# Kernel optimization log

Measured on AMD Instinct MI355X. Metric: run time of the kernel, lower is better.

Reference implementation:

```python
import jax, jax.numpy as jnp
import numpy as np

N_NODES = 100000


def _sage_conv(x, src, dst, W_l, b, W_r):
    """PyG SAGEConv with mean aggregation: lin_l(mean_{j in N(i)} x_j) + lin_r(x_i).
    edge_index[0]=src (message source j), edge_index[1]=dst (target i)."""
    n = x.shape[0]
    # sum of neighbor features per target node, then divide by in-degree
    agg = jax.ops.segment_sum(x[src], dst, num_segments=n)  # [N, F]
    deg = jax.ops.segment_sum(jnp.ones_like(dst, dtype=x.dtype), dst, num_segments=n)
    agg = agg / jnp.maximum(deg, 1.0)[:, None]
    return agg @ W_l + b + x @ W_r


def setup_inputs() -> dict:
    key = jax.random.key(0)
    ks = jax.random.split(key, 8)
    in_c, hid, out = 128, 128, 2
    sc = lambda f: 1.0 / np.sqrt(f)
    x = jax.random.normal(ks[0], (N_NODES, in_c), dtype=jnp.float32)
    edge_index = jax.random.randint(ks[1], (2, 1600000), 0, N_NODES, dtype=jnp.int64)
    return {
        "x": x,
        "edge_index": edge_index,
        "W1_l": jax.random.normal(ks[2], (in_c, hid), dtype=jnp.float32) * sc(in_c),
        "b1": jnp.zeros((hid,), dtype=jnp.float32),
        "W1_r": jax.random.normal(ks[3], (in_c, hid), dtype=jnp.float32) * sc(in_c),
        "W2_l": jax.random.normal(ks[4], (hid, hid), dtype=jnp.float32) * sc(hid),
        "b2": jnp.zeros((hid,), dtype=jnp.float32),
        "W2_r": jax.random.normal(ks[5], (hid, hid), dtype=jnp.float32) * sc(hid),
        "W_fc": jax.random.normal(ks[6], (hid, out), dtype=jnp.float32) * sc(hid),
        "b_fc": jnp.zeros((out,), dtype=jnp.float32),
    }


def reference(x, edge_index, W1_l, b1, W1_r, W2_l, b2, W2_r, W_fc, b_fc):
    src, dst = edge_index[0], edge_index[1]
    # eval mode: dropout is identity
    h = jax.nn.relu(_sage_conv(x, src, dst, W1_l, b1, W1_r))
    h = jax.nn.relu(_sage_conv(h, src, dst, W2_l, b2, W2_r))
    return h @ W_fc + b_fc
```

## Files before the change

kernel.cpp:

```cpp
#include <hip/hip_runtime.h>

#define NF 128
#define SH 9
#define BNODES 512
#define MAXNB 256

typedef unsigned short u16;
typedef unsigned int u32;
using u16x4 = __attribute__((ext_vector_type(4))) u16;
using u16x8 = __attribute__((ext_vector_type(8))) u16;
using s16x8 = __attribute__((ext_vector_type(8))) short;
using f32x4 = __attribute__((ext_vector_type(4))) float;
using u32x4 = __attribute__((ext_vector_type(4))) u32;
using i32x4 = __attribute__((ext_vector_type(4))) int;

__device__ inline float b2f(u16 b) {
    union { u32 u; float f; } c; c.u = (u32)b << 16; return c.f;
}
__device__ inline u16 f2b(float f) {
    union { float f; u32 u; } c; c.f = f;
    u32 u = c.u;
    u += 0x7FFFu + ((u >> 16) & 1u);
    return (u16)(u >> 16);
}
__device__ inline u16x8 nt_load8(const u16* p) {
    u32x4 v = __builtin_nontemporal_load((const u32x4*)p);
    return *(u16x8*)&v;
}
__device__ inline void nt_store8(u16* p, u16x8 v) {
    __builtin_nontemporal_store(*(u32x4*)&v, (u32x4*)p);
}
__device__ inline int padded4(int d) { return (d + 3) & ~3; }

__global__ __launch_bounds__(256) void bhist_kernel(const int* __restrict__ dst,
                                                    int* __restrict__ bcnt, int E, int NB) {
    __shared__ int h[MAXNB];
    int t = threadIdx.x;
    h[t] = 0;
    __syncthreads();
    for (int e = blockIdx.x * 256 + t; e < E; e += gridDim.x * 256)
        atomicAdd(&h[__builtin_nontemporal_load(dst + e) >> SH], 1);
    __syncthreads();
    if (t < NB && h[t]) atomicAdd(&bcnt[t], h[t]);
}

__global__ __launch_bounds__(256) void bscan_kernel(const int* __restrict__ bcnt,
                                                    int* __restrict__ boff,
                                                    int* __restrict__ gcur, int NB, int E) {
    __shared__ int ss[256];
    int t = threadIdx.x;
    int v = (t < NB) ? bcnt[t] : 0;
    ss[t] = v; __syncthreads();
    for (int off = 1; off < 256; off <<= 1) {
        int u = (t >= off) ? ss[t - off] : 0;
        __syncthreads();
        ss[t] += u;
        __syncthreads();
    }
    int excl = ss[t] - v;
    if (t < NB) { boff[t] = excl; gcur[t] = excl; }
    if (t == 0) boff[NB] = E;
}

__global__ __launch_bounds__(256) void scatter_kernel(
    const int* __restrict__ src, const int* __restrict__ dst,
    int* __restrict__ gcur, u32* __restrict__ pairs, int E, int NB)
{
    __shared__ int hist[MAXNB];
    __shared__ int cstart[256];
    __shared__ int gbase[MAXNB];
    __shared__ u32 stage[4096];
    __shared__ u16 bmap[4096];
    int t = threadIdx.x;
    int base = blockIdx.x * 4096;

    hist[t] = 0;
    __syncthreads();

    u32 packed[16]; int bb[16]; int loff[16];
    #pragma unroll
    for (int j = 0; j < 16; j++) {
        int e = base + j * 256 + t;
        bb[j] = -1;
        if (e < E) {
            int d = __builtin_nontemporal_load(dst + e);
            int s = __builtin_nontemporal_load(src + e);
            int b = d >> SH;
            bb[j] = b;
            packed[j] = ((u32)(d & (BNODES - 1)) << 17) | (u32)s;
            loff[j] = atomicAdd(&hist[b], 1);
        }
    }
    __syncthreads();

    int hv = hist[t];
    cstart[t] = hv; __syncthreads();
    for (int off = 1; off < 256; off <<= 1) {
        int u = (t >= off) ? cstart[t - off] : 0;
        __syncthreads();
        cstart[t] += u;
        __syncthreads();
    }
    int excl = cstart[t] - hv;
    if (t < NB && hv > 0) gbase[t] = atomicAdd(&gcur[t], hv);
    __syncthreads();
    cstart[t] = excl;
    __syncthreads();

    #pragma unroll
    for (int j = 0; j < 16; j++) if (bb[j] >= 0) {
        int pos = cstart[bb[j]] + loff[j];
        stage[pos] = packed[j];
        bmap[pos] = (u16)bb[j];
    }
    __syncthreads();

    int total = min(4096, E - base);
    for (int k = t; k < total; k += 256) {
        u32 p = stage[k];
        int b = bmap[k];
        pairs[gbase[b] + (k - cstart[b])] = p;
    }
}

__global__ __launch_bounds__(256) void degb_kernel(const u32* __restrict__ pairs,
                                                   const int* __restrict__ boff,
                                                   int* __restrict__ deg, int n) {
    __shared__ int dl[BNODES];
    int b = blockIdx.x, t = threadIdx.x;
    for (int i = t; i < BNODES; i += 256) dl[i] = 0;
    __syncthreads();
    int s = boff[b], e = boff[b + 1];
    for (int k = s + t; k < e; k += 256)
        atomicAdd(&dl[__builtin_nontemporal_load(pairs + k) >> 17], 1);
    __syncthreads();
    int nb0 = b << SH;
    for (int i = t; i < BNODES; i += 256)
        if (nb0 + i < n) deg[nb0 + i] = dl[i];
}

__global__ __launch_bounds__(256) void scanA_kernel(const int* __restrict__ deg,
                                                    int* __restrict__ bsum, int n) {
    __shared__ int red[256];
    int t = threadIdx.x;
    int i0 = blockIdx.x * 1024 + t * 4;
    int s = 0;
    if (i0 + 3 < n) {
        int4 d = *(const int4*)(deg + i0);
        s = padded4(d.x) + padded4(d.y) + padded4(d.z) + padded4(d.w);
    } else {
        for (int j = 0; j < 4; j++) if (i0 + j < n) s += padded4(deg[i0 + j]);
    }
    red[t] = s; __syncthreads();
    for (int off = 128; off; off >>= 1) {
        if (t < off) red[t] += red[t + off];
        __syncthreads();
    }
    if (!t) bsum[blockIdx.x] = red[0];
}

__global__ __launch_bounds__(128) void scanB_kernel(int* __restrict__ bsum, int nb) {
    __shared__ int ss[128];
    int t = threadIdx.x;
    int v = (t < nb) ? bsum[t] : 0;
    ss[t] = v; __syncthreads();
    for (int off = 1; off < 128; off <<= 1) {
        int u = (t >= off) ? ss[t - off] : 0;
        __syncthreads();
        ss[t] += u;
        __syncthreads();
    }
    if (t < nb) bsum[t] = ss[t] - v;
}

__global__ __launch_bounds__(256) void scanC_kernel(const int* __restrict__ deg,
                                                    const int* __restrict__ bsum,
                                                    int* __restrict__ info,
                                                    int* __restrict__ adj, int n) {
    __shared__ int ss[256];
    int t = threadIdx.x;
    int i0 = blockIdx.x * 1024 + t * 4;
    int4 d = make_int4(0, 0, 0, 0);
    if (i0 + 3 < n) d = *(const int4*)(deg + i0);
    else {
        if (i0     < n) d.x = deg[i0];
        if (i0 + 1 < n) d.y = deg[i0 + 1];
        if (i0 + 2 < n) d.z = deg[i0 + 2];
        if (i0 + 3 < n) d.w = deg[i0 + 3];
    }
    int px = padded4(d.x), py = padded4(d.y), pz = padded4(d.z), pw = padded4(d.w);
    int s = px + py + pz + pw;
    ss[t] = s; __syncthreads();
    for (int off = 1; off < 256; off <<= 1) {
        int u = (t >= off) ? ss[t - off] : 0;
        __syncthreads();
        ss[t] += u;
        __syncthreads();
    }
    int b0 = bsum[blockIdx.x] + ss[t] - s;
    int b1 = b0 + px, b2 = b1 + py, b3 = b2 + pz;
    if (i0 + 3 < n) {
        i32x4 w0 = {b0, d.x, b1, d.y};
        i32x4 w1 = {b2, d.z, b3, d.w};
        ((i32x4*)info)[i0 / 2]     = w0;
        ((i32x4*)info)[i0 / 2 + 1] = w1;
    } else {
        if (i0     < n) { info[2 * i0]     = b0; info[2 * i0 + 1] = d.x; }
        if (i0 + 1 < n) { info[2 * i0 + 2] = b1; info[2 * i0 + 3] = d.y; }
        if (i0 + 2 < n) { info[2 * i0 + 4] = b2; info[2 * i0 + 5] = d.z; }
        if (i0 + 3 < n) { info[2 * i0 + 6] = b3; info[2 * i0 + 7] = d.w; }
    }
    if (i0     < n) for (int p = d.x; p < px; p++) adj[b0 + p] = n;
    if (i0 + 1 < n) for (int p = d.y; p < py; p++) adj[b1 + p] = n;
    if (i0 + 2 < n) for (int p = d.z; p < pz; p++) adj[b2 + p] = n;
    if (i0 + 3 < n) for (int p = d.w; p < pw; p++) adj[b3 + p] = n;
}

__global__ __launch_bounds__(256) void fill2_kernel(const u32* __restrict__ pairs,
                                                    const int* __restrict__ boff,
                                                    const int* __restrict__ info,
                                                    int* __restrict__ adj, int n) {
    __shared__ int begl[BNODES];
    __shared__ int curl[BNODES];
    int b = blockIdx.x, t = threadIdx.x;
    int nb0 = b << SH;
    for (int i = t; i < BNODES; i += 256) {
        int nd = nb0 + i;
        if (nd < n) begl[i] = info[2 * nd];
        curl[i] = 0;
    }
    __syncthreads();
    int s = boff[b], e = boff[b + 1];
    for (int k = s + t; k < e; k += 256) {
        u32 p = __builtin_nontemporal_load(pairs + k);
        int ld = p >> 17, sr = p & 0x1FFFF;
        int pos = atomicAdd(&curl[ld], 1);
        adj[begl[ld] + pos] = sr;
    }
}

__global__ __launch_bounds__(256) void cast_x_kernel(const float* __restrict__ x,
                                                     u16* __restrict__ xb, int n, int nr) {
    int i = blockIdx.x * 256 + threadIdx.x;
    if (i >= nr * (NF / 8)) return;
    int node = i >> 4, ch = i & 15;
    u16x8 o = (u16x8)0;
    if (node < n) {
        const float* p = x + (size_t)node * NF + ch * 8;
        f32x4 v0 = __builtin_nontemporal_load((const f32x4*)p);
        f32x4 v1 = __builtin_nontemporal_load((const f32x4*)(p + 4));
        o[0] = f2b(v0[0]); o[1] = f2b(v0[1]); o[2] = f2b(v0[2]); o[3] = f2b(v0[3]);
        o[4] = f2b(v1[0]); o[5] = f2b(v1[1]); o[6] = f2b(v1[2]); o[7] = f2b(v1[3]);
    }
    *(u16x8*)(xb + (size_t)node * NF + ch * 8) = o;
}

__global__ void cast_wt_kernel(const float* __restrict__ w0, const float* __restrict__ w1,
                               const float* __restrict__ w2, const float* __restrict__ w3,
                               u16* __restrict__ o0, u16* __restrict__ o1,
                               u16* __restrict__ o2, u16* __restrict__ o3) {
    int m = blockIdx.y;
    const float* w = (m == 0) ? w0 : (m == 1) ? w1 : (m == 2) ? w2 : w3;
    u16* o = (m == 0) ? o0 : (m == 1) ? o1 : (m == 2) ? o2 : o3;
    int i = blockIdx.x * 256 + threadIdx.x;
    int k = i >> 7, nc = i & 127;
    o[nc * NF + k] = f2b(w[k * NF + nc]);
}

__global__ __launch_bounds__(256) void gather_kernel(
    const u16* __restrict__ xb,
    const int* __restrict__ info,
    const int* __restrict__ adj,
    u16* __restrict__ agg,
    int n)
{
    int node = blockIdx.x * 16 + (threadIdx.x >> 4);
    if (node >= n) return;
    int lane = threadIdx.x & 15;
    const u16* xs = xb + lane * 8;

    int2 inf = *(const int2*)(info + 2 * node);
    int beg = inf.x, deg = inf.y;
    const i32x4* ap = (const i32x4*)(adj + beg);
    int ng = (deg + 3) >> 2;

    float a[8];
    #pragma unroll
    for (int j = 0; j < 8; j++) a[j] = 0.f;

#define ROW(nb) (*(const u16x8*)(xs + (size_t)(nb) * NF))

    i32x4 ia, ib;
    if (ng >= 2) {
        ia = __builtin_nontemporal_load(ap);
        ib = __builtin_nontemporal_load(ap + 1);
    }
    int g = 0;
    while (g + 2 <= ng) {
        i32x4 ca = ia, cb = ib;
        g += 2;
        if (g + 2 <= ng) {
            ia = __builtin_nontemporal_load(ap + g);
            ib = __builtin_nontemporal_load(ap + g + 1);
        }
        u16x8 v0 = ROW(ca[0]), v1 = ROW(ca[1]), v2 = ROW(ca[2]), v3 = ROW(ca[3]);
        u16x8 v4 = ROW(cb[0]), v5 = ROW(cb[1]), v6 = ROW(cb[2]), v7 = ROW(cb[3]);
        #pragma unroll
        for (int j = 0; j < 8; j++)
            a[j] += ((b2f(v0[j]) + b2f(v1[j])) + (b2f(v2[j]) + b2f(v3[j])))
                  + ((b2f(v4[j]) + b2f(v5[j])) + (b2f(v6[j]) + b2f(v7[j])));
    }
    if (g < ng) {
        i32x4 ca = __builtin_nontemporal_load(ap + g);
        u16x8 v0 = ROW(ca[0]), v1 = ROW(ca[1]), v2 = ROW(ca[2]), v3 = ROW(ca[3]);
        #pragma unroll
        for (int j = 0; j < 8; j++)
            a[j] += (b2f(v0[j]) + b2f(v1[j])) + (b2f(v2[j]) + b2f(v3[j]));
    }
#undef ROW

    float invd = 1.0f / fmaxf((float)deg, 1.0f);
    u16x8 o;
    #pragma unroll
    for (int j = 0; j < 8; j++) o[j] = f2b(a[j] * invd);
    *(u16x8*)(agg + (size_t)node * NF + lane * 8) = o;
}

template <bool FC>
__global__ __launch_bounds__(256) void sage_mfma_kernel(
    const u16* __restrict__ agg,
    const u16* __restrict__ selfb,
    const u16* __restrict__ Wtl,
    const u16* __restrict__ Wtr,
    const float* __restrict__ bias,
    const float* __restrict__ Wfc,
    const float* __restrict__ bfc,
    u16* __restrict__ hout,
    float* __restrict__ out,
    int n)
{
    constexpr int MT = 64;
    constexpr int LDK = 136;
    __shared__ u16 A_s[MT][LDK];
    __shared__ u16 W_s[NF][LDK];

    int t = threadIdx.x;
    int node0 = blockIdx.x * MT;

    #pragma unroll
    for (int i = 0; i < 8; i++) {
        int idx = t + i * 256;
        int row = idx >> 4, ch = idx & 15;
        *(u16x8*)&W_s[row][ch * 8] = ((const u16x8*)Wtl)[row * 16 + ch];
    }
    #pragma unroll
    for (int i = 0; i < 4; i++) {
        int idx = t + i * 256;
        int row = idx >> 4, ch = idx & 15;
        int node = node0 + row;
        u16x8 v = (u16x8)0;
        if (node < n) v = nt_load8(agg + (size_t)node * NF + ch * 8);
        *(u16x8*)&A_s[row][ch * 8] = v;
    }
    __syncthreads();

    int l = t & 63;
    int lr = l & 15;
    int lko = (l >> 4) * 8;
    int m0 = (t >> 6) * 16;

    f32x4 acc[8];
    #pragma unroll
    for (int f = 0; f < 8; f++) acc[f] = (f32x4)0.f;

    #pragma unroll
    for (int ks = 0; ks < NF; ks += 32) {
        s16x8 a = *(const s16x8*)&A_s[m0 + lr][ks + lko];
        #pragma unroll
        for (int f = 0; f < 8; f++) {
            s16x8 b = *(const s16x8*)&W_s[f * 16 + lr][ks + lko];
            acc[f] = __builtin_amdgcn_mfma_f32_16x16x32_bf16(a, b, acc[f], 0, 0, 0);
        }
    }
    __syncthreads();

    #pragma unroll
    for (int i = 0; i < 8; i++) {
        int idx = t + i * 256;
        int row = idx >> 4, ch = idx & 15;
        *(u16x8*)&W_s[row][ch * 8] = ((const u16x8*)Wtr)[row * 16 + ch];
    }
    #pragma unroll
    for (int i = 0; i < 4; i++) {
        int idx = t + i * 256;
        int row = idx >> 4, ch = idx & 15;
        int node = node0 + row;
        u16x8 v = (u16x8)0;
        if (node < n) v = nt_load8(selfb + (size_t)node * NF + ch * 8);
        *(u16x8*)&A_s[row][ch * 8] = v;
    }
    __syncthreads();

    #pragma unroll
    for (int ks = 0; ks < NF; ks += 32) {
        s16x8 a = *(const s16x8*)&A_s[m0 + lr][ks + lko];
        #pragma unroll
        for (int f = 0; f < 8; f++) {
            s16x8 b = *(const s16x8*)&W_s[f * 16 + lr][ks + lko];
            acc[f] = __builtin_amdgcn_mfma_f32_16x16x32_bf16(a, b, acc[f], 0, 0, 0);
        }
    }

    __syncthreads();
    int rowb = m0 + (l >> 4) * 4;
    #pragma unroll
    for (int f = 0; f < 8; f++) {
        float bc = bias[f * 16 + lr];
        #pragma unroll
        for (int r = 0; r < 4; r++) {
            float v = fmaxf(acc[f][r] + bc, 0.f);
            A_s[rowb + r][f * 16 + lr] = f2b(v);
        }
    }
    __syncthreads();

    if (!FC) {
        #pragma unroll
        for (int i = 0; i < 4; i++) {
            int idx = t + i * 256;
            int row = idx >> 4, ch = idx & 15;
            int node = node0 + row;
            if (node < n)
                nt_store8(hout + (size_t)node * NF + ch * 8, *(u16x8*)&A_s[row][ch * 8]);
            else if (node == n)
                nt_store8(hout + (size_t)node * NF + ch * 8, (u16x8)0);
        }
    } else {
        int g = t >> 5, lane = t & 31;
        float2 wfc[4];
        #pragma unroll
        for (int j = 0; j < 4; j++) wfc[j] = ((const float2*)Wfc)[lane * 4 + j];
        float bf0 = bfc[0], bf1 = bfc[1];
        for (int m8 = 0; m8 < 8; m8++) {
            int m = g * 8 + m8;
            float p0 = 0.f, p1 = 0.f;
            #pragma unroll
            for (int j = 0; j < 4; j++) {
                float h = b2f(A_s[m][lane * 4 + j]);
                p0 += h * wfc[j].x;
                p1 += h * wfc[j].y;
            }
            #pragma unroll
            for (int s = 16; s; s >>= 1) {
                p0 += __shfl_down(p0, s, 32);
                p1 += __shfl_down(p1, s, 32);
            }
            int node = node0 + m;
            if (lane == 0 && node < n)
                *(float2*)(out + (size_t)node * 2) = make_float2(p0 + bf0, p1 + bf1);
        }
    }
}

extern "C" void kernel_launch(void* const* d_in, const int* in_sizes, int n_in,
                              void* d_out, int out_size, void* d_ws, size_t ws_size,
                              hipStream_t stream) {
    const float* x   = (const float*)d_in[0];
    const int*   ei  = (const int*)d_in[1];
    const float* W1l = (const float*)d_in[2];
    const float* b1  = (const float*)d_in[3];
    const float* W1r = (const float*)d_in[4];
    const float* W2l = (const float*)d_in[5];
    const float* b2  = (const float*)d_in[6];
    const float* W2r = (const float*)d_in[7];
    const float* Wfc = (const float*)d_in[8];
    const float* bfc = (const float*)d_in[9];

    const int n = in_sizes[0] / NF;
    const int E = in_sizes[1] / 2;
    const int nr = n + 1;
    const int NB = (n + BNODES - 1) >> SH;
    const int* src = ei;
    const int* dst = ei + E;

    u16* xb     = (u16*)d_ws;
    u16* agg    = xb  + (size_t)nr * NF;
    u16* h1     = agg + (size_t)nr * NF;
    u16* Wt1l   = h1  + (size_t)nr * NF;
    u16* Wt1r   = Wt1l + NF * NF;
    u16* Wt2l   = Wt1r + NF * NF;
    u16* Wt2r   = Wt2l + NF * NF;
    int* adj    = (int*)(Wt2r + NF * NF);
    int* deg    = adj + ((size_t)E + 3 * (size_t)n);
    int* info   = deg + n;
    int* bsum   = info + 2 * (size_t)n;
    int* bcnt   = bsum + 128;
    int* gcur   = bcnt + 256;
    int* boff   = gcur + 256;
    u32* pairs  = (u32*)(boff + 257);

    (void)hipMemsetAsync(bcnt, 0, 512 * sizeof(int), stream);

    bhist_kernel<<<1024, 256, 0, stream>>>(dst, bcnt, E, NB);
    bscan_kernel<<<1, 256, 0, stream>>>(bcnt, boff, gcur, NB, E);
    scatter_kernel<<<(E + 4095) / 4096, 256, 0, stream>>>(src, dst, gcur, pairs, E, NB);
    degb_kernel<<<NB, 256, 0, stream>>>(pairs, boff, deg, n);

    int nbA = (n + 1023) / 1024;
    scanA_kernel<<<nbA, 256, 0, stream>>>(deg, bsum, n);
    scanB_kernel<<<1, 128, 0, stream>>>(bsum, nbA);
    scanC_kernel<<<nbA, 256, 0, stream>>>(deg, bsum, info, adj, n);
    fill2_kernel<<<NB, 256, 0, stream>>>(pairs, boff, info, adj, n);

    cast_x_kernel<<<(nr * (NF / 8) + 255) / 256, 256, 0, stream>>>(x, xb, n, nr);
    cast_wt_kernel<<<dim3(64, 4), 256, 0, stream>>>(W1l, W1r, W2l, W2r,
                                                    Wt1l, Wt1r, Wt2l, Wt2r);

    int gb = (n + 15) / 16;
    int cb = (nr + 63) / 64;
    gather_kernel<<<gb, 256, 0, stream>>>(xb, info, adj, agg, n);
    sage_mfma_kernel<false><<<cb, 256, 0, stream>>>(
        agg, xb, Wt1l, Wt1r, b1, nullptr, nullptr, h1, nullptr, n);
    gather_kernel<<<gb, 256, 0, stream>>>(h1, info, adj, agg, n);
    sage_mfma_kernel<true><<<cb, 256, 0, stream>>>(
        agg, h1, Wt2l, Wt2r, b2, Wfc, bfc, nullptr, (float*)d_out, n);
}
```

Before: 268.5 us.

## Fuse neighbor mean-gather into the SAGE MFMA kernel and drop the agg buffer

```diff
diff --git a/kernel.cpp b/kernel.cpp
--- a/kernel.cpp
+++ b/kernel.cpp
@@ -16,6 +16,12 @@
 
 __device__ inline float b2f(u16 b) {
     union { u32 u; float f; } c; c.u = (u32)b << 16; return c.f;
+}
+__device__ inline float lo2f(u32 w) {
+    union { u32 u; float f; } c; c.u = w << 16; return c.f;
+}
+__device__ inline float hi2f(u32 w) {
+    union { u32 u; float f; } c; c.u = w & 0xFFFF0000u; return c.f;
 }
 __device__ inline u16 f2b(float f) {
     union { float f; u32 u; } c; c.f = f;
@@ -267,69 +273,11 @@
     o[nc * NF + k] = f2b(w[k * NF + nc]);
 }
 
-__global__ __launch_bounds__(256) void gather_kernel(
-    const u16* __restrict__ xb,
+template <bool FC>
+__global__ __launch_bounds__(512) void sage_fused_kernel(
+    const u16* __restrict__ xin,
     const int* __restrict__ info,
     const int* __restrict__ adj,
-    u16* __restrict__ agg,
-    int n)
-{
-    int node = blockIdx.x * 16 + (threadIdx.x >> 4);
-    if (node >= n) return;
-    int lane = threadIdx.x & 15;
-    const u16* xs = xb + lane * 8;
-
-    int2 inf = *(const int2*)(info + 2 * node);
-    int beg = inf.x, deg = inf.y;
-    const i32x4* ap = (const i32x4*)(adj + beg);
-    int ng = (deg + 3) >> 2;
-
-    float a[8];
-    #pragma unroll
-    for (int j = 0; j < 8; j++) a[j] = 0.f;
-
-#define ROW(nb) (*(const u16x8*)(xs + (size_t)(nb) * NF))
-
-    i32x4 ia, ib;
-    if (ng >= 2) {
-        ia = __builtin_nontemporal_load(ap);
-        ib = __builtin_nontemporal_load(ap + 1);
-    }
-    int g = 0;
-    while (g + 2 <= ng) {
-        i32x4 ca = ia, cb = ib;
-        g += 2;
-        if (g + 2 <= ng) {
-            ia = __builtin_nontemporal_load(ap + g);
-            ib = __builtin_nontemporal_load(ap + g + 1);
-        }
-        u16x8 v0 = ROW(ca[0]), v1 = ROW(ca[1]), v2 = ROW(ca[2]), v3 = ROW(ca[3]);
-        u16x8 v4 = ROW(cb[0]), v5 = ROW(cb[1]), v6 = ROW(cb[2]), v7 = ROW(cb[3]);
-        #pragma unroll
-        for (int j = 0; j < 8; j++)
-            a[j] += ((b2f(v0[j]) + b2f(v1[j])) + (b2f(v2[j]) + b2f(v3[j])))
-                  + ((b2f(v4[j]) + b2f(v5[j])) + (b2f(v6[j]) + b2f(v7[j])));
-    }
-    if (g < ng) {
-        i32x4 ca = __builtin_nontemporal_load(ap + g);
-        u16x8 v0 = ROW(ca[0]), v1 = ROW(ca[1]), v2 = ROW(ca[2]), v3 = ROW(ca[3]);
-        #pragma unroll
-        for (int j = 0; j < 8; j++)
-            a[j] += (b2f(v0[j]) + b2f(v1[j])) + (b2f(v2[j]) + b2f(v3[j]));
-    }
-#undef ROW
-
-    float invd = 1.0f / fmaxf((float)deg, 1.0f);
-    u16x8 o;
-    #pragma unroll
-    for (int j = 0; j < 8; j++) o[j] = f2b(a[j] * invd);
-    *(u16x8*)(agg + (size_t)node * NF + lane * 8) = o;
-}
-
-template <bool FC>
-__global__ __launch_bounds__(256) void sage_mfma_kernel(
-    const u16* __restrict__ agg,
-    const u16* __restrict__ selfb,
     const u16* __restrict__ Wtl,
     const u16* __restrict__ Wtr,
     const float* __restrict__ bias,
@@ -339,7 +287,7 @@
     float* __restrict__ out,
     int n)
 {
-    constexpr int MT = 64;
+    constexpr int MT = 128;
     constexpr int LDK = 136;
     __shared__ u16 A_s[MT][LDK];
     __shared__ u16 W_s[NF][LDK];
@@ -348,19 +296,68 @@
     int node0 = blockIdx.x * MT;
 
     #pragma unroll
-    for (int i = 0; i < 8; i++) {
-        int idx = t + i * 256;
+    for (int i = 0; i < 4; i++) {
+        int idx = t + i * 512;
         int row = idx >> 4, ch = idx & 15;
         *(u16x8*)&W_s[row][ch * 8] = ((const u16x8*)Wtl)[row * 16 + ch];
     }
-    #pragma unroll
-    for (int i = 0; i < 4; i++) {
-        int idx = t + i * 256;
-        int row = idx >> 4, ch = idx & 15;
-        int node = node0 + row;
-        u16x8 v = (u16x8)0;
-        if (node < n) v = nt_load8(agg + (size_t)node * NF + ch * 8);
-        *(u16x8*)&A_s[row][ch * 8] = v;
+
+    {
+        int grp = t >> 4, lane = t & 15;
+        const char* xbase = (const char*)xin;
+        u32 lo16 = (u32)lane * 16;
+
+        for (int j = 0; j < 4; j++) {
+            int m = grp * 4 + j;
+            int node = node0 + m;
+            float L[4] = {0.f, 0.f, 0.f, 0.f}, H[4] = {0.f, 0.f, 0.f, 0.f};
+            int dg = 0;
+            if (node < n) {
+                int2 inf = *(const int2*)(info + 2 * node);
+                dg = inf.y;
+                const i32x4* ap = (const i32x4*)(adj + inf.x);
+                int ng = (dg + 3) >> 2;
+
+#define ROWU(nb) (*(const u32x4*)(xbase + (((u32)(nb) << 8) + lo16)))
+#define ACC4(cur) { \
+    u32x4 r0 = ROWU(cur[0]), r1 = ROWU(cur[1]), r2 = ROWU(cur[2]), r3 = ROWU(cur[3]); \
+    _Pragma("unroll") \
+    for (int k = 0; k < 4; k++) { \
+        L[k] += (lo2f(r0[k]) + lo2f(r1[k])) + (lo2f(r2[k]) + lo2f(r3[k])); \
+        H[k] += (hi2f(r0[k]) + hi2f(r1[k])) + (hi2f(r2[k]) + hi2f(r3[k])); \
+    } }
+                i32x4 ia, ib;
+                if (ng >= 2) {
+                    ia = __builtin_nontemporal_load(ap);
+                    ib = __builtin_nontemporal_load(ap + 1);
+                }
+                int g = 0;
+                while (g + 2 <= ng) {
+                    i32x4 ca = ia, cb = ib;
+                    g += 2;
+                    if (g + 2 <= ng) {
+                        ia = __builtin_nontemporal_load(ap + g);
+                        ib = __builtin_nontemporal_load(ap + g + 1);
+                    }
+                    ACC4(ca);
+                    ACC4(cb);
+                }
+                if (g < ng) {
+                    i32x4 ca = __builtin_nontemporal_load(ap + g);
+                    ACC4(ca);
+                }
+#undef ACC4
+#undef ROWU
+            }
+            float invd = 1.0f / fmaxf((float)dg, 1.0f);
+            u16x8 o;
+            #pragma unroll
+            for (int k = 0; k < 4; k++) {
+                o[2 * k]     = f2b(L[k] * invd);
+                o[2 * k + 1] = f2b(H[k] * invd);
+            }
+            *(u16x8*)&A_s[m][lane * 8] = o;
+        }
     }
     __syncthreads();
 
@@ -385,18 +382,18 @@
     __syncthreads();
 
     #pragma unroll
-    for (int i = 0; i < 8; i++) {
-        int idx = t + i * 256;
+    for (int i = 0; i < 4; i++) {
+        int idx = t + i * 512;
         int row = idx >> 4, ch = idx & 15;
         *(u16x8*)&W_s[row][ch * 8] = ((const u16x8*)Wtr)[row * 16 + ch];
     }
     #pragma unroll
     for (int i = 0; i < 4; i++) {
-        int idx = t + i * 256;
+        int idx = t + i * 512;
         int row = idx >> 4, ch = idx & 15;
         int node = node0 + row;
         u16x8 v = (u16x8)0;
-        if (node < n) v = nt_load8(selfb + (size_t)node * NF + ch * 8);
+        if (node < n) v = nt_load8(xin + (size_t)node * NF + ch * 8);
         *(u16x8*)&A_s[row][ch * 8] = v;
     }
     __syncthreads();
@@ -427,7 +424,7 @@
     if (!FC) {
         #pragma unroll
         for (int i = 0; i < 4; i++) {
-            int idx = t + i * 256;
+            int idx = t + i * 512;
             int row = idx >> 4, ch = idx & 15;
             int node = node0 + row;
             if (node < n)
@@ -484,9 +481,8 @@
     const int* dst = ei + E;
 
     u16* xb     = (u16*)d_ws;
-    u16* agg    = xb  + (size_t)nr * NF;
-    u16* h1     = agg + (size_t)nr * NF;
-    u16* Wt1l   = h1  + (size_t)nr * NF;
+    u16* h1     = xb + (size_t)nr * NF;
+    u16* Wt1l   = h1 + (size_t)nr * NF;
     u16* Wt1r   = Wt1l + NF * NF;
     u16* Wt2l   = Wt1r + NF * NF;
     u16* Wt2r   = Wt2l + NF * NF;
@@ -516,12 +512,9 @@
     cast_wt_kernel<<<dim3(64, 4), 256, 0, stream>>>(W1l, W1r, W2l, W2r,
                                                     Wt1l, Wt1r, Wt2l, Wt2r);
 
-    int gb = (n + 15) / 16;
-    int cb = (nr + 63) / 64;
-    gather_kernel<<<gb, 256, 0, stream>>>(xb, info, adj, agg, n);
-    sage_mfma_kernel<false><<<cb, 256, 0, stream>>>(
-        agg, xb, Wt1l, Wt1r, b1, nullptr, nullptr, h1, nullptr, n);
-    gather_kernel<<<gb, 256, 0, stream>>>(h1, info, adj, agg, n);
-    sage_mfma_kernel<true><<<cb, 256, 0, stream>>>(
-        agg, h1, Wt2l, Wt2r, b2, Wfc, bfc, nullptr, (float*)d_out, n);
-}
+    int fb = (nr + 127) / 128;
+    sage_fused_kernel<false><<<fb, 512, 0, stream>>>(
+        xb, info, adj, Wt1l, Wt1r, b1, nullptr, nullptr, h1, nullptr, n);
+    sage_fused_kernel<true><<<fb, 512, 0, stream>>>(
+        h1, info, adj, Wt2l, Wt2r, b2, Wfc, bfc, nullptr, (float*)d_out, n);
+}
```

New measurement: 265.2 us. No clear change (-1.2%).
